# Kernel tuning notes

Hardware: AMD Instinct MI355X
Metric: run time of the kernel (lower is better)

## Reference

```python
import jax, jax.numpy as jnp
import numpy as np

GRID_SIZE = 5
SPLINE_ORDER = 3
K = 3  # conv kernel size
_H = 2.0 / GRID_SIZE
# grid points: (arange(-order, grid_size+order+1) * h + grid_range[0]) -> [-2.2, ..., 2.2], 12 pts
GRID = jnp.arange(-SPLINE_ORDER, GRID_SIZE + SPLINE_ORDER + 1, dtype=jnp.float32) * _H - 1.0


def b_splines(x):
    """Cox-de Boor B-spline bases. x: [N, in] -> [N, in, grid_size+order]."""
    g = GRID
    xg = x[..., None]  # [N, in, 1]
    bases = ((xg >= g[:-1]) & (xg < g[1:])).astype(x.dtype)  # order-0 indicators
    for k in range(1, SPLINE_ORDER + 1):
        left = (xg - g[:-(k + 1)]) / (g[k:-1] - g[:-(k + 1)]) * bases[..., :-1]
        right = (g[k + 1:] - xg) / (g[k + 1:] - g[1:-k]) * bases[..., 1:]
        bases = left + right
    return bases  # [N, in, 8]


def setup_inputs() -> dict:
    key = jax.random.key(0)
    ks = jax.random.split(key, 6)
    B, C, H, W = 8, 1, 512, 512
    n_convs, in_feat, n_coef = 16, K * K, GRID_SIZE + SPLINE_ORDER
    x = jax.random.normal(ks[0], (B, C, H, W), dtype=jnp.float32)
    base_weight = jax.random.normal(ks[1], (n_convs, in_feat), dtype=jnp.float32) / np.sqrt(in_feat)
    spline_weight = jax.random.normal(ks[2], (n_convs, in_feat, n_coef), dtype=jnp.float32) * 0.1
    spline_scaler = jax.random.normal(ks[3], (n_convs, in_feat), dtype=jnp.float32) / np.sqrt(in_feat)
    restore_w = jax.random.normal(ks[4], (1, n_convs, K, K), dtype=jnp.float32) / np.sqrt(n_convs * K * K)
    restore_b = jax.random.normal(ks[5], (1,), dtype=jnp.float32) * 0.01
    return {"x": x, "base_weight": base_weight, "spline_weight": spline_weight,
            "spline_scaler": spline_scaler, "restore_w": restore_w, "restore_b": restore_b}


def reference(x, base_weight, spline_weight, spline_scaler, restore_w, restore_b):
    B, C, H, W = x.shape  # C == 1
    # im2col: [B, 9, H, W] (padding 1 preserves spatial dims)
    patches = jax.lax.conv_general_dilated_patches(
        x, (K, K), (1, 1), padding=((1, 1), (1, 1)))
    p = patches.transpose(0, 2, 3, 1).reshape(-1, K * K)  # [N, 9], N = B*H*W
    # KANLinear applied per patch, vectorized over all n_convs (shared grid -> shared bases)
    sp = b_splines(p)  # [N, 9, 8]
    base_out = jnp.einsum('ni,ci->nc', jax.nn.silu(p), base_weight)
    scaled_w = spline_weight * spline_scaler[..., None]  # [n_convs, 9, 8]
    spline_out = jnp.einsum('nio,cio->nc', sp, scaled_w)
    feat = (base_out + spline_out).reshape(B, H, W, -1).transpose(0, 3, 1, 2)  # [B, n_convs, H, W]
    # restore: standard Conv2d(n_convs -> 1, 3x3, padding 1)
    out = jax.lax.conv_general_dilated(
        feat, restore_w, (1, 1), ((1, 1), (1, 1)),
        dimension_numbers=('NCHW', 'OIHW', 'NCHW'))
    return out + restore_b[None, :, None, None]
```

## Files before the change

### kernel.cpp

```cpp
#include <hip/hip_runtime.h>
#include <math.h>

#define IMG_H 512
#define IMG_W 512
#define NBATCH 8
#define TILE 32
#define GDIM 36
#define NCH 9
#define NCONV 16
#define NPOS (GDIM * GDIM)
#define RINGN (2 * (IMG_W + 2) + 2 * IMG_H)
#define CPB 16

#define WOFF_WCH 0
#define WOFF_WCS 128
#define WOFF_W1 256

typedef _Float16 h2 __attribute__((ext_vector_type(2)));
typedef _Float16 h8 __attribute__((ext_vector_type(8)));

__device__ __forceinline__ void eval_gb(float x, float& sl, float bj[8]) {
    float u = fmaf(x, 2.5f, 5.5f);
    float fi = floorf(u);
    int i = (int)fi;
    float t = u - fi;
    float s1 = 1.f - t;
    float t2 = t * t, t3 = t2 * t;
    float w0 = s1 * s1 * s1 * (1.f / 6.f);
    float w3 = t3 * (1.f / 6.f);
    float w1v = fmaf(0.5f, t3, 2.f / 3.f) - t2;
    float msk = (u >= 0.f && u < 11.f) ? 1.f : 0.f;
    w0 *= msk; w1v *= msk; w3 *= msk;
    float w2v = msk - w0 - w1v - w3;
    sl = x / (1.f + __expf(-x));
#pragma unroll
    for (int j = 0; j < 8; ++j) {
        float v = 0.f;
        v = (i == j)     ? w3  : v;
        v = (i == j + 1) ? w2v : v;
        v = (i == j + 2) ? w1v : v;
        v = (i == j + 3) ? w0  : v;
        bj[j] = v;
    }
}

__device__ __forceinline__ void eval_g(float x, float g[NCH]) {
    float sl, bj[8];
    eval_gb(x, sl, bj);
    g[0] = sl;
#pragma unroll
    for (int j = 0; j < 8; ++j) g[j + 1] = bj[j];
}

__device__ __forceinline__ void ring2fyfx(int r, int& fy, int& fx) {
    if (r < IMG_W + 2)            { fy = -1;    fx = r - 1; }
    else if (r < 2 * (IMG_W + 2)) { fy = IMG_H; fx = (r - (IMG_W + 2)) - 1; }
    else if (r < 2 * (IMG_W + 2) + IMG_H) { fy = r - 2 * (IMG_W + 2); fx = -1; }
    else                          { fy = r - (2 * (IMG_W + 2) + IMG_H); fx = IMG_W; }
}

__global__ void ConvKAN_prep(const float* __restrict__ bw, const float* __restrict__ sw,
                             const float* __restrict__ ss, const float* __restrict__ rw,
                             float* __restrict__ ws) {
    __shared__ float WC[225];
    int t = threadIdx.x;
    for (int idx = t; idx < NCONV * 9 * NCH; idx += 256) {
        int ci = idx / NCH;
        int ch = idx % NCH;
        ws[WOFF_W1 + idx] = (ch == 0) ? bw[ci] : sw[ci * 8 + (ch - 1)] * ss[ci];
    }
    if (t < 225) {
        int de = t / NCH, ch = t % NCH;
        int d = de / 5, e = de % 5;
        float s = 0.0f;
        for (int c = 0; c < NCONV; ++c) {
            int ulo = d - 2 > 0 ? d - 2 : 0, uhi = d < 2 ? d : 2;
            int vlo = e - 2 > 0 ? e - 2 : 0, vhi = e < 2 ? e : 2;
            for (int u = ulo; u <= uhi; ++u)
                for (int v = vlo; v <= vhi; ++v) {
                    int i = (d - u) * 3 + (e - v);
                    float w1v = (ch == 0) ? bw[c * 9 + i]
                                          : sw[(c * 9 + i) * 8 + (ch - 1)] * ss[c * 9 + i];
                    s += rw[c * 9 + u * 3 + v] * w1v;
                }
        }
        WC[t] = s;
    }
    __syncthreads();
    if (t < 25) {
        h8 hw;
#pragma unroll
        for (int j = 0; j < 8; ++j) hw[j] = (_Float16)WC[t * 9 + 1 + j];
        ((h8*)(ws + WOFF_WCH))[t] = hw;
        ws[WOFF_WCS + t] = WC[t * 9];
    }
}

__global__ __launch_bounds__(256) void ConvKAN_main(const float* __restrict__ x,
                                                    const float* __restrict__ wpack,
                                                    const float* __restrict__ wsl,
                                                    const float* __restrict__ rb,
                                                    float* __restrict__ out) {
    __shared__ h8 HB[NPOS];
    __shared__ float SS[NPOS];
    int tid = threadIdx.x;
    int b = blockIdx.z;
    int y0 = blockIdx.y * TILE, x0 = blockIdx.x * TILE;
    const float* xb = x + (size_t)b * IMG_H * IMG_W;

    for (int i = tid; i < NPOS; i += 256) {
        int r = i / GDIM, c = i % GDIM;
        int gy = y0 + r - 2, gx = x0 + c - 2;
        float xv = (gy >= 0 && gy < IMG_H && gx >= 0 && gx < IMG_W) ? xb[gy * IMG_W + gx] : 0.0f;
        float sl, bj[8];
        eval_gb(xv, sl, bj);
        h8 hv;
#pragma unroll
        for (int j = 0; j < 8; ++j) hv[j] = (_Float16)bj[j];
        HB[i] = hv; SS[i] = sl;
    }
    __syncthreads();

    int tx = tid & 31;
    int ty = tid >> 5;
    int r0 = ty * 4;
    float bias = rb[0];
    float acc[4] = {bias, bias, bias, bias};

#pragma unroll
    for (int R = 0; R < 8; ++R) {
#pragma unroll
        for (int e = 0; e < 5; ++e) {
            int pos = (r0 + R) * GDIM + tx + e;
            h8 hv = HB[pos]; float sl = SS[pos];
            h2 b0 = {hv[0], hv[1]}, b1 = {hv[2], hv[3]};
            h2 b2 = {hv[4], hv[5]}, b3 = {hv[6], hv[7]};
#pragma unroll
            for (int p = 0; p < 4; ++p) {
                int d = R - p;
                if (d < 0 || d > 4) continue;
                int t = d * 5 + e;
                const h2* wh = (const h2*)&wpack[t * 4];
                float a0 = fmaf(sl, wsl[t], acc[p]);
                a0 = __builtin_amdgcn_fdot2(b0, wh[0], a0, false);
                a0 = __builtin_amdgcn_fdot2(b1, wh[1], a0, false);
                a0 = __builtin_amdgcn_fdot2(b2, wh[2], a0, false);
                a0 = __builtin_amdgcn_fdot2(b3, wh[3], a0, false);
                acc[p] = a0;
            }
        }
    }
    float* ob = out + ((size_t)b * IMG_H + y0) * IMG_W + x0;
#pragma unroll
    for (int p = 0; p < 4; ++p)
        ob[(r0 + p) * IMG_W + tx] = acc[p];
}

__global__ __launch_bounds__(256) void ConvKAN_corr(const float* __restrict__ x,
        const float* __restrict__ w1, const float* __restrict__ rw,
        float* __restrict__ out) {
    __shared__ float LW[NCONV * 81];
    __shared__ float G[CPB * 81];

    int tid = threadIdx.x;
    for (int idx = tid; idx < NCONV * 81; idx += 256) LW[idx] = w1[idx];

    if (tid < CPB * 9) {
        int pl = tid / 9, tap = tid % 9;
        int pg = blockIdx.x * CPB + pl;
        int b = pg / RINGN, r = pg % RINGN;
        int fy, fx;
        ring2fyfx(r, fy, fx);
        int a = tap / 3, bb = tap % 3;
        int gy = fy + a - 1, gx = fx + bb - 1;
        const float* xb = x + (size_t)b * IMG_H * IMG_W;
        float xv = (gy >= 0 && gy < IMG_H && gx >= 0 && gx < IMG_W) ? xb[gy * IMG_W + gx] : 0.f;
        float g[NCH];
        eval_g(xv, g);
#pragma unroll
        for (int ch = 0; ch < NCH; ++ch) G[pl * 81 + tap * 9 + ch] = g[ch];
    }
    __syncthreads();

    int pl = tid >> 4, c = tid & 15;
    int pg = blockIdx.x * CPB + pl;
    int b = pg / RINGN, r = pg % RINGN;
    int fy, fx;
    ring2fyfx(r, fy, fx);

    float fc = 0.f;
#pragma unroll
    for (int i = 0; i < 9; ++i)
#pragma unroll
        for (int ch = 0; ch < 9; ++ch)
            fc = fmaf(LW[c * 81 + i * 9 + ch], G[pl * 81 + i * 9 + ch], fc);

#pragma unroll
    for (int dd = 0; dd < 9; ++dd) {
        int u = dd / 3, v = dd % 3;
        int ty = fy - (u - 1), tx2 = fx - (v - 1);
        if (ty >= 0 && ty < IMG_H && tx2 >= 0 && tx2 < IMG_W) {
            float s = rw[c * 9 + dd] * fc;
            s += __shfl_xor(s, 1);
            s += __shfl_xor(s, 2);
            s += __shfl_xor(s, 4);
            s += __shfl_xor(s, 8);
            if (c == 0)
                atomicAdd(&out[((size_t)b * IMG_H + ty) * IMG_W + tx2], -s);
        }
    }
}

extern "C" void kernel_launch(void* const* d_in, const int* in_sizes, int n_in,
                              void* d_out, int out_size, void* d_ws, size_t ws_size,
                              hipStream_t stream) {
    const float* x  = (const float*)d_in[0];
    const float* bw = (const float*)d_in[1];
    const float* sw = (const float*)d_in[2];
    const float* ss = (const float*)d_in[3];
    const float* rw = (const float*)d_in[4];
    const float* rb = (const float*)d_in[5];
    float* out = (float*)d_out;
    float* ws  = (float*)d_ws;

    ConvKAN_prep<<<1, 256, 0, stream>>>(bw, sw, ss, rw, ws);
    ConvKAN_main<<<dim3(IMG_W / TILE, IMG_H / TILE, NBATCH), 256, 0, stream>>>(
        x, ws + WOFF_WCH, ws + WOFF_WCS, rb, out);
    int nblk = (NBATCH * RINGN) / CPB;
    ConvKAN_corr<<<nblk, 256, 0, stream>>>(x, ws + WOFF_W1, rw, out);
}
```

Before: 125.9 us.

## Restructure border correction as per-output-pixel gather with folded restore weights

Result: no change. 125.3 us (-0.5%).

```diff
diff --git a/kernel.cpp b/kernel.cpp
--- a/kernel.cpp
+++ b/kernel.cpp
@@ -9,12 +9,11 @@
 #define NCH 9
 #define NCONV 16
 #define NPOS (GDIM * GDIM)
-#define RINGN (2 * (IMG_W + 2) + 2 * IMG_H)
-#define CPB 16
+#define NBORD (2 * IMG_W + 2 * (IMG_H - 2))
 
 #define WOFF_WCH 0
 #define WOFF_WCS 128
-#define WOFF_W1 256
+#define WOFF_WV  256
 
 typedef _Float16 h2 __attribute__((ext_vector_type(2)));
 typedef _Float16 h8 __attribute__((ext_vector_type(8)));
@@ -52,23 +51,18 @@
     for (int j = 0; j < 8; ++j) g[j + 1] = bj[j];
 }
 
-__device__ __forceinline__ void ring2fyfx(int r, int& fy, int& fx) {
-    if (r < IMG_W + 2)            { fy = -1;    fx = r - 1; }
-    else if (r < 2 * (IMG_W + 2)) { fy = IMG_H; fx = (r - (IMG_W + 2)) - 1; }
-    else if (r < 2 * (IMG_W + 2) + IMG_H) { fy = r - 2 * (IMG_W + 2); fx = -1; }
-    else                          { fy = r - (2 * (IMG_W + 2) + IMG_H); fx = IMG_W; }
-}
-
 __global__ void ConvKAN_prep(const float* __restrict__ bw, const float* __restrict__ sw,
                              const float* __restrict__ ss, const float* __restrict__ rw,
                              float* __restrict__ ws) {
+    __shared__ float W1s[NCONV * 81];
     __shared__ float WC[225];
     int t = threadIdx.x;
-    for (int idx = t; idx < NCONV * 9 * NCH; idx += 256) {
+    for (int idx = t; idx < NCONV * 81; idx += 256) {
         int ci = idx / NCH;
         int ch = idx % NCH;
-        ws[WOFF_W1 + idx] = (ch == 0) ? bw[ci] : sw[ci * 8 + (ch - 1)] * ss[ci];
-    }
+        W1s[idx] = (ch == 0) ? bw[ci] : sw[ci * 8 + (ch - 1)] * ss[ci];
+    }
+    __syncthreads();
     if (t < 225) {
         int de = t / NCH, ch = t % NCH;
         int d = de / 5, e = de % 5;
@@ -79,12 +73,17 @@
             for (int u = ulo; u <= uhi; ++u)
                 for (int v = vlo; v <= vhi; ++v) {
                     int i = (d - u) * 3 + (e - v);
-                    float w1v = (ch == 0) ? bw[c * 9 + i]
-                                          : sw[(c * 9 + i) * 8 + (ch - 1)] * ss[c * 9 + i];
-                    s += rw[c * 9 + u * 3 + v] * w1v;
+                    s += rw[c * 9 + u * 3 + v] * W1s[(c * 9 + i) * NCH + ch];
                 }
         }
         WC[t] = s;
+    }
+    for (int idx = t; idx < 729; idx += 256) {
+        int uv = idx / 81, rest = idx % 81;
+        float s = 0.f;
+        for (int c = 0; c < NCONV; ++c)
+            s += rw[c * 9 + uv] * W1s[c * 81 + rest];
+        ws[WOFF_WV + idx] = s;
     }
     __syncthreads();
     if (t < 25) {
@@ -157,58 +156,42 @@
 }
 
 __global__ __launch_bounds__(256) void ConvKAN_corr(const float* __restrict__ x,
-        const float* __restrict__ w1, const float* __restrict__ rw,
-        float* __restrict__ out) {
-    __shared__ float LW[NCONV * 81];
-    __shared__ float G[CPB * 81];
-
+        const float* __restrict__ wv, float* __restrict__ out) {
+    __shared__ float WV[729];
     int tid = threadIdx.x;
-    for (int idx = tid; idx < NCONV * 81; idx += 256) LW[idx] = w1[idx];
-
-    if (tid < CPB * 9) {
-        int pl = tid / 9, tap = tid % 9;
-        int pg = blockIdx.x * CPB + pl;
-        int b = pg / RINGN, r = pg % RINGN;
-        int fy, fx;
-        ring2fyfx(r, fy, fx);
-        int a = tap / 3, bb = tap % 3;
-        int gy = fy + a - 1, gx = fx + bb - 1;
-        const float* xb = x + (size_t)b * IMG_H * IMG_W;
-        float xv = (gy >= 0 && gy < IMG_H && gx >= 0 && gx < IMG_W) ? xb[gy * IMG_W + gx] : 0.f;
-        float g[NCH];
-        eval_g(xv, g);
-#pragma unroll
-        for (int ch = 0; ch < NCH; ++ch) G[pl * 81 + tap * 9 + ch] = g[ch];
-    }
-    __syncthreads();
-
-    int pl = tid >> 4, c = tid & 15;
-    int pg = blockIdx.x * CPB + pl;
-    int b = pg / RINGN, r = pg % RINGN;
-    int fy, fx;
-    ring2fyfx(r, fy, fx);
-
-    float fc = 0.f;
-#pragma unroll
-    for (int i = 0; i < 9; ++i)
-#pragma unroll
-        for (int ch = 0; ch < 9; ++ch)
-            fc = fmaf(LW[c * 81 + i * 9 + ch], G[pl * 81 + i * 9 + ch], fc);
-
-#pragma unroll
-    for (int dd = 0; dd < 9; ++dd) {
-        int u = dd / 3, v = dd % 3;
-        int ty = fy - (u - 1), tx2 = fx - (v - 1);
-        if (ty >= 0 && ty < IMG_H && tx2 >= 0 && tx2 < IMG_W) {
-            float s = rw[c * 9 + dd] * fc;
-            s += __shfl_xor(s, 1);
-            s += __shfl_xor(s, 2);
-            s += __shfl_xor(s, 4);
-            s += __shfl_xor(s, 8);
-            if (c == 0)
-                atomicAdd(&out[((size_t)b * IMG_H + ty) * IMG_W + tx2], -s);
+    for (int idx = tid; idx < 729; idx += 256) WV[idx] = wv[idx];
+    __syncthreads();
+
+    int q = blockIdx.x * 256 + tid;
+    if (q >= NBATCH * NBORD) return;
+    int b = q / NBORD, r = q % NBORD;
+    int y, xc;
+    if (r < IMG_W)               { y = 0;             xc = r; }
+    else if (r < 2 * IMG_W)      { y = IMG_H - 1;     xc = r - IMG_W; }
+    else if (r < 2 * IMG_W + IMG_H - 2) { y = r - 2 * IMG_W + 1; xc = 0; }
+    else                         { y = r - (2 * IMG_W + IMG_H - 2) + 1; xc = IMG_W - 1; }
+
+    const float* xb = x + (size_t)b * IMG_H * IMG_W;
+    float corr = 0.f;
+#pragma unroll 1
+    for (int uv = 0; uv < 9; ++uv) {
+        int du = uv / 3 - 1, dv = uv % 3 - 1;
+        int fy = y + du, fx = xc + dv;
+        if (fy >= 0 && fy < IMG_H && fx >= 0 && fx < IMG_W) continue;
+        const float* wvp = &WV[uv * 81];
+#pragma unroll
+        for (int tap = 0; tap < 9; ++tap) {
+            int gy = fy + tap / 3 - 1, gx = fx + tap % 3 - 1;
+            float xv = (gy >= 0 && gy < IMG_H && gx >= 0 && gx < IMG_W) ? xb[gy * IMG_W + gx] : 0.f;
+            float g[NCH];
+            eval_g(xv, g);
+#pragma unroll
+            for (int ch = 0; ch < NCH; ++ch)
+                corr = fmaf(wvp[tap * 9 + ch], g[ch], corr);
         }
     }
+    size_t oi = ((size_t)b * IMG_H + y) * IMG_W + xc;
+    out[oi] = out[oi] - corr;
 }
 
 extern "C" void kernel_launch(void* const* d_in, const int* in_sizes, int n_in,
@@ -226,6 +209,6 @@
     ConvKAN_prep<<<1, 256, 0, stream>>>(bw, sw, ss, rw, ws);
     ConvKAN_main<<<dim3(IMG_W / TILE, IMG_H / TILE, NBATCH), 256, 0, stream>>>(
         x, ws + WOFF_WCH, ws + WOFF_WCS, rb, out);
-    int nblk = (NBATCH * RINGN) / CPB;
-    ConvKAN_corr<<<nblk, 256, 0, stream>>>(x, ws + WOFF_W1, rw, out);
-}
+    int nthr = NBATCH * NBORD;
+    ConvKAN_corr<<<(nthr + 255) / 256, 256, 0, stream>>>(x, ws + WOFF_WV, out);
+}
```
